# Kernel optimization log

Hardware: AMD Instinct MI355X
Metric: run time of the kernel (lower is better)

## Reference

```python
import jax, jax.numpy as jnp
import numpy as np

N_QUBITS = 16
REPS = 2
BATCH = 512


def _apply_1q_batched(state, gates, q):
    """Apply per-sample 2x2 gates [B,2,2] to qubit q of state [B]+[2]*n."""
    state = jnp.moveaxis(state, 1 + q, -1)
    state = jnp.einsum('bij,b...j->b...i', gates, state)
    return jnp.moveaxis(state, -1, 1 + q)


def _apply_1q(state, gate, q):
    """Apply a shared 2x2 gate to qubit q of state [B]+[2]*n."""
    state = jnp.moveaxis(state, 1 + q, -1)
    state = jnp.einsum('ij,b...j->b...i', gate, state)
    return jnp.moveaxis(state, -1, 1 + q)


def _apply_cnot(state, c, t):
    """CNOT with control c, target t on state [B]+[2]*n."""
    state = jnp.moveaxis(state, (1 + c, 1 + t), (-2, -1))
    state = jnp.stack([state[..., 0, :], state[..., 1, ::-1]], axis=-2)
    return jnp.moveaxis(state, (-2, -1), (1 + c, 1 + t))


def _rx_gates(theta):
    """RX(theta) gates; theta [...,] -> gates [...,2,2] complex64."""
    c = jnp.cos(theta / 2).astype(jnp.complex64)
    s = (-1j * jnp.sin(theta / 2)).astype(jnp.complex64)
    row0 = jnp.stack([c, s], axis=-1)
    row1 = jnp.stack([s, c], axis=-1)
    return jnp.stack([row0, row1], axis=-2)


def _pauliz_signs(n):
    idx = np.arange(2 ** n)
    # pennylane convention: wire 0 is the most significant bit
    bits = (idx[None, :] >> (n - 1 - np.arange(n)[:, None])) & 1  # [n, 2^n]
    return jnp.asarray(1.0 - 2.0 * bits, dtype=jnp.float32)


def setup_inputs() -> dict:
    key = jax.random.key(0)
    kz, kp, kw = jax.random.split(key, 3)
    z = jax.random.normal(kz, (BATCH, N_QUBITS), dtype=jnp.float32)
    params = jax.random.normal(kp, (N_QUBITS,), dtype=jnp.float32) * 0.1
    ent_weights = jax.random.normal(kw, (REPS, N_QUBITS), dtype=jnp.float32) * 0.1
    return {"z": z, "params": params, "ent_weights": ent_weights}


def reference(z, params, ent_weights):
    B, n = z.shape
    # |0...0> initial state, batched
    state = jnp.zeros((B, 2 ** n), dtype=jnp.complex64).at[:, 0].set(1.0)
    state = state.reshape([B] + [2] * n)

    # Embedding layer: RX(z[b,i] + params[i]) on each wire (per-sample angles)
    angles = z + params[None, :]  # [B, n]
    for q in range(n):
        state = _apply_1q_batched(state, _rx_gates(angles[:, q]), q)

    # BasicEntanglerLayers, reps=2: per layer, RX(w) on each wire then ring CNOTs
    for l in range(REPS):
        for q in range(n):
            state = _apply_1q(state, _rx_gates(ent_weights[l, q]), q)
        for q in range(n):
            state = _apply_cnot(state, q, (q + 1) % n)

    # <Z_i> for each wire
    probs = jnp.abs(state.reshape(B, -1)) ** 2  # [B, 2^n] float32
    signs = _pauliz_signs(n)  # [n, 2^n]
    return probs @ signs.T  # [B, n]
```

## Files before the change

kernel.cpp:

```cpp
#include <hip/hip_runtime.h>

#define NQ 16

__device__ __forceinline__ float2 phase_val(float mag, int k) {
    switch (k & 3) {
        case 0:  return make_float2(mag, 0.f);
        case 1:  return make_float2(0.f, -mag);
        case 2:  return make_float2(-mag, 0.f);
        default: return make_float2(0.f, mag);
    }
}

extern "C" __global__ __launch_bounds__(256)
void qsim_kernel(const float* __restrict__ z,
                 const float* __restrict__ params,
                 const float* __restrict__ ew,
                 float* __restrict__ out)
{
    const int b   = blockIdx.x;
    const int tid = threadIdx.x;

    __shared__ float c1[NQ], s1[NQ], cw[NQ], sw[NQ];
    __shared__ float2 V[8][256];
    __shared__ float2 G[2][9][10];

    if (tid < NQ) {
        float phi = z[b * NQ + tid] + params[tid] + ew[tid];
        c1[tid] = cosf(0.5f * phi);
        s1[tid] = sinf(0.5f * phi);
        float w = 0.5f * ew[NQ + tid];
        cw[tid] = cosf(w);
        sw[tid] = sinf(w);
    }
    __syncthreads();

    {
        const int h = tid;
        int y[8];
#pragma unroll
        for (int q = 0; q < 8; ++q) y[q] = (h >> (7 - q)) & 1;

        float2 A[2];
#pragma unroll
        for (int t = 0; t < 2; ++t) {
            float mag = 1.f; int k = 0;
            int e = y[0] ^ t;          mag *= e ? s1[0] : c1[0]; k += e;
            e = y[1] ^ y[0] ^ t;       mag *= e ? s1[1] : c1[1]; k += e;
#pragma unroll
            for (int q = 2; q < 8; ++q) { e = y[q - 1] ^ y[q]; mag *= e ? s1[q] : c1[q]; k += e; }
            A[t] = phase_val(mag, k);
        }
        const int a_act = h & 1;
        V[2 * a_act + 0][h] = A[0];
        V[2 * a_act + 1][h] = A[1];
        V[2 * (1 - a_act) + 0][h] = make_float2(0.f, 0.f);
        V[2 * (1 - a_act) + 1][h] = make_float2(0.f, 0.f);

        float2 Bv[2];
#pragma unroll
        for (int a = 0; a < 2; ++a) {
            float mag = 1.f; int k = 0;
            int e = a ^ y[0];          mag *= e ? s1[8] : c1[8]; k += e;
#pragma unroll
            for (int q = 9; q < 16; ++q) { e = y[q - 9] ^ y[q - 8]; mag *= e ? s1[q] : c1[q]; k += e; }
            Bv[a] = phase_val(mag, k);
        }
        const int b_act = h & 1;
        V[4 + 0 + b_act][h] = Bv[0];
        V[4 + 2 + b_act][h] = Bv[1];
        V[4 + 0 + (1 - b_act)][h] = make_float2(0.f, 0.f);
        V[4 + 2 + (1 - b_act)][h] = make_float2(0.f, 0.f);
    }
    __syncthreads();

    for (int j = 0; j < 8; ++j) {
        const int bit = 7 - j;
#pragma unroll
        for (int r = 0; r < 4; ++r) {
            int task = tid + 256 * r;
            int vec  = task >> 7;
            int pr   = task & 127;
            int h0 = ((pr >> bit) << (bit + 1)) | (pr & ((1 << bit) - 1));
            int h1 = h0 | (1 << bit);
            int wire = (vec < 4) ? j : (8 + j);
            float c = cw[wire], s = sw[wire];
            float2 v0 = V[vec][h0], v1 = V[vec][h1];
            float2 n0 = make_float2(c * v0.x + s * v1.y, c * v0.y - s * v1.x);
            float2 n1 = make_float2(s * v0.y + c * v1.x, -s * v0.x + c * v1.y);
            V[vec][h0] = n0;
            V[vec][h1] = n1;
        }
        __syncthreads();
    }

    if (tid < 180) {
        int side = tid / 90;
        int rest = tid - side * 90;
        int pp   = rest / 9;
        int m    = rest - pp * 9;
        int p, q2;
        if (pp < 4)      { p = 0; q2 = pp; }
        else if (pp < 7) { p = 1; q2 = pp - 3; }
        else if (pp < 9) { p = 2; q2 = pp - 5; }
        else             { p = 3; q2 = 3; }
        int mask;
        if (side == 0) mask = (m < 8) ? (((1 << (m + 1)) - 1) << (7 - m)) : 0x7F;
        else           mask = (m == 0) ? 0 : (((1 << m) - 1) << (8 - m));
        const float2* Vp = V[p  + 4 * side];
        const float2* Vq = V[q2 + 4 * side];
        float ar = 0.f, ai = 0.f;
        for (int e2 = 0; e2 < 256; ++e2) {
            float2 u = Vp[e2], w = Vq[e2];
            float re = u.x * w.x + u.y * w.y;
            float im = u.y * w.x - u.x * w.y;
            float sgn = (__popc(mask & e2) & 1) ? -1.f : 1.f;
            ar = fmaf(sgn, re, ar);
            ai = fmaf(sgn, im, ai);
        }
        G[side][m][pp] = make_float2(ar, ai);
    }
    __syncthreads();

    if (tid < NQ) {
        const int i = tid;
        int hm, lm;
        if (i == 0)      { hm = 8; lm = 8; }
        else if (i <= 7) { hm = i; lm = 0; }
        else             { hm = 7; lm = i - 7; }
        float r = 0.f;
#pragma unroll
        for (int pp = 0; pp < 10; ++pp) {
            float2 gh = G[0][hm][pp];
            float2 gl = G[1][lm][pp];
            float re = gh.x * gl.x - gh.y * gl.y;
            bool diag = (pp == 0) || (pp == 4) || (pp == 7) || (pp == 9);
            r += (diag ? 1.f : 2.f) * re;
        }
        out[b * NQ + i] = r;
    }
}

extern "C" void kernel_launch(void* const* d_in, const int* in_sizes, int n_in,
                              void* d_out, int out_size, void* d_ws, size_t ws_size,
                              hipStream_t stream) {
    const float* z      = (const float*)d_in[0];
    const float* params = (const float*)d_in[1];
    const float* ew     = (const float*)d_in[2];
    float* out          = (float*)d_out;
    const int B = in_sizes[0] / NQ;
    qsim_kernel<<<B, 256, 0, stream>>>(z, params, ew, out);
}
```

Before: 73.21 us.

## Keep state in registers with wave shuffles and use Walsh-Hadamard butterflies for Gram sums

The per-wire RX mixing now runs in registers using wave shuffles instead of shared-memory passes with a barrier after each wire. Only the last wire goes through shared memory via float4 loads. The old 180-thread serial 256-element signed Gram reduction is replaced by an in-register signed butterfly across lanes (a Walsh-Hadamard-style transform). Each wave writes a few partial sums to shared memory, and a small final pass combines them. This removes most barriers and the long serial reduction loops, at the cost of heavier register use (a 32-float array per thread plus many shuffles).

```diff
diff --git a/kernel.cpp b/kernel.cpp
--- a/kernel.cpp
+++ b/kernel.cpp
@@ -11,17 +11,24 @@
     }
 }
 
+__device__ __forceinline__ float2 rxmix(float2 v0, float2 v1, float c, float s) {
+    return make_float2(c * v0.x + s * v1.y, c * v0.y - s * v1.x);
+}
+
 extern "C" __global__ __launch_bounds__(256)
 void qsim_kernel(const float* __restrict__ z,
                  const float* __restrict__ params,
                  const float* __restrict__ ew,
                  float* __restrict__ out)
 {
-    const int b   = blockIdx.x;
-    const int tid = threadIdx.x;
+    const int b    = blockIdx.x;
+    const int tid  = threadIdx.x;
+    const int lane = tid & 63;
+    const int wv   = tid >> 6;
 
     __shared__ float c1[NQ], s1[NQ], cw[NQ], sw[NQ];
-    __shared__ float2 V[8][256];
+    __shared__ __align__(16) float2 V4[4][258];
+    __shared__ __align__(16) float  PART[4][7][32];
     __shared__ float2 G[2][9][10];
 
     if (tid < NQ) {
@@ -34,90 +41,189 @@
     }
     __syncthreads();
 
-    {
-        const int h = tid;
-        int y[8];
-#pragma unroll
-        for (int q = 0; q < 8; ++q) y[q] = (h >> (7 - q)) & 1;
-
-        float2 A[2];
-#pragma unroll
-        for (int t = 0; t < 2; ++t) {
-            float mag = 1.f; int k = 0;
-            int e = y[0] ^ t;          mag *= e ? s1[0] : c1[0]; k += e;
-            e = y[1] ^ y[0] ^ t;       mag *= e ? s1[1] : c1[1]; k += e;
-#pragma unroll
-            for (int q = 2; q < 8; ++q) { e = y[q - 1] ^ y[q]; mag *= e ? s1[q] : c1[q]; k += e; }
-            A[t] = phase_val(mag, k);
-        }
-        const int a_act = h & 1;
-        V[2 * a_act + 0][h] = A[0];
-        V[2 * a_act + 1][h] = A[1];
-        V[2 * (1 - a_act) + 0][h] = make_float2(0.f, 0.f);
-        V[2 * (1 - a_act) + 1][h] = make_float2(0.f, 0.f);
-
-        float2 Bv[2];
-#pragma unroll
-        for (int a = 0; a < 2; ++a) {
-            float mag = 1.f; int k = 0;
-            int e = a ^ y[0];          mag *= e ? s1[8] : c1[8]; k += e;
-#pragma unroll
-            for (int q = 9; q < 16; ++q) { e = y[q - 9] ^ y[q - 8]; mag *= e ? s1[q] : c1[q]; k += e; }
-            Bv[a] = phase_val(mag, k);
-        }
-        const int b_act = h & 1;
-        V[4 + 0 + b_act][h] = Bv[0];
-        V[4 + 2 + b_act][h] = Bv[1];
-        V[4 + 0 + (1 - b_act)][h] = make_float2(0.f, 0.f);
-        V[4 + 2 + (1 - b_act)][h] = make_float2(0.f, 0.f);
-    }
-    __syncthreads();
-
-    for (int j = 0; j < 8; ++j) {
-        const int bit = 7 - j;
-#pragma unroll
-        for (int r = 0; r < 4; ++r) {
-            int task = tid + 256 * r;
-            int vec  = task >> 7;
-            int pr   = task & 127;
-            int h0 = ((pr >> bit) << (bit + 1)) | (pr & ((1 << bit) - 1));
-            int h1 = h0 | (1 << bit);
-            int wire = (vec < 4) ? j : (8 + j);
-            float c = cw[wire], s = sw[wire];
-            float2 v0 = V[vec][h0], v1 = V[vec][h1];
-            float2 n0 = make_float2(c * v0.x + s * v1.y, c * v0.y - s * v1.x);
-            float2 n1 = make_float2(s * v0.y + c * v1.x, -s * v0.x + c * v1.y);
-            V[vec][h0] = n0;
-            V[vec][h1] = n1;
-        }
-        __syncthreads();
-    }
+    const bool hiw = (wv < 2);
+    const int  par = wv & 1;
+
+    float2 v[4];
+#pragma unroll
+    for (int k = 0; k < 4; ++k) {
+        int e = (k << 6) | lane;
+        float mag = 1.f; int kk = 0;
+        if (hiw) {
+            int y0 = (e >> 7) & 1;
+            int eb = y0 ^ par;                 mag *= eb ? s1[0] : c1[0]; kk += eb;
+            int y1 = (e >> 6) & 1;
+            eb = y1 ^ y0 ^ par;                mag *= eb ? s1[1] : c1[1]; kk += eb;
+            int yp = y1;
+#pragma unroll
+            for (int q = 2; q < 8; ++q) {
+                int yq = (e >> (7 - q)) & 1;
+                eb = yp ^ yq;                  mag *= eb ? s1[q] : c1[q]; kk += eb;
+                yp = yq;
+            }
+        } else {
+            int yp = (e >> 7) & 1;
+            int eb = par ^ yp;                 mag *= eb ? s1[8] : c1[8]; kk += eb;
+#pragma unroll
+            for (int q = 9; q < 16; ++q) {
+                int yq = (e >> (15 - q)) & 1;
+                eb = yp ^ yq;                  mag *= eb ? s1[q] : c1[q]; kk += eb;
+                yp = yq;
+            }
+        }
+        v[k] = phase_val(mag, kk);
+    }
+
+    const int wb = hiw ? 0 : 8;
+    {
+        float c = cw[wb + 0], s = sw[wb + 0];
+        float2 n0 = rxmix(v[0], v[2], c, s), n2 = rxmix(v[2], v[0], c, s);
+        float2 n1 = rxmix(v[1], v[3], c, s), n3 = rxmix(v[3], v[1], c, s);
+        v[0] = n0; v[1] = n1; v[2] = n2; v[3] = n3;
+    }
+    {
+        float c = cw[wb + 1], s = sw[wb + 1];
+        float2 n0 = rxmix(v[0], v[1], c, s), n1 = rxmix(v[1], v[0], c, s);
+        float2 n2 = rxmix(v[2], v[3], c, s), n3 = rxmix(v[3], v[2], c, s);
+        v[0] = n0; v[1] = n1; v[2] = n2; v[3] = n3;
+    }
+#pragma unroll
+    for (int bbit = 5; bbit >= 1; --bbit) {
+        float c = cw[wb + 7 - bbit], s = sw[wb + 7 - bbit];
+        int m = 1 << bbit;
+#pragma unroll
+        for (int k = 0; k < 4; ++k) {
+            float px = __shfl_xor(v[k].x, m);
+            float py = __shfl_xor(v[k].y, m);
+            v[k] = make_float2(c * v[k].x + s * py, c * v[k].y - s * px);
+        }
+    }
+#pragma unroll
+    for (int k = 0; k < 4; ++k) V4[wv][(k << 6) | lane] = v[k];
+    __syncthreads();
+
+    const int e0 = tid & 1, j2 = tid & ~1;
+    float4 rA0 = *(const float4*)&V4[0][j2];
+    float4 rA1 = *(const float4*)&V4[1][j2];
+    float4 rB0 = *(const float4*)&V4[2][j2];
+    float4 rB1 = *(const float4*)&V4[3][j2];
+    float c7 = cw[7], s7 = sw[7], c15 = cw[15], s15 = sw[15];
+
+    float2 x[4], yv[4];
+    {
+        float2 a0 = make_float2(rA0.x, rA0.y), b0 = make_float2(rA0.z, rA0.w);
+        float2 a1 = make_float2(rA1.x, rA1.y), b1 = make_float2(rA1.z, rA1.w);
+        if (e0 == 0) {
+            x[0] = make_float2(c7 * a0.x, c7 * a0.y);
+            x[1] = make_float2(c7 * a1.x, c7 * a1.y);
+            x[2] = make_float2(s7 * b0.y, -s7 * b0.x);
+            x[3] = make_float2(s7 * b1.y, -s7 * b1.x);
+        } else {
+            x[0] = make_float2(s7 * a0.y, -s7 * a0.x);
+            x[1] = make_float2(s7 * a1.y, -s7 * a1.x);
+            x[2] = make_float2(c7 * b0.x, c7 * b0.y);
+            x[3] = make_float2(c7 * b1.x, c7 * b1.y);
+        }
+        float2 g0 = make_float2(rB0.x, rB0.y), d0 = make_float2(rB0.z, rB0.w);
+        float2 g1 = make_float2(rB1.x, rB1.y), d1 = make_float2(rB1.z, rB1.w);
+        if (e0 == 0) {
+            yv[0] = make_float2(c15 * g0.x, c15 * g0.y);
+            yv[2] = make_float2(c15 * g1.x, c15 * g1.y);
+            yv[1] = make_float2(s15 * d0.y, -s15 * d0.x);
+            yv[3] = make_float2(s15 * d1.y, -s15 * d1.x);
+        } else {
+            yv[0] = make_float2(s15 * g0.y, -s15 * g0.x);
+            yv[2] = make_float2(s15 * g1.y, -s15 * g1.x);
+            yv[1] = make_float2(c15 * d0.x, c15 * d0.y);
+            yv[3] = make_float2(c15 * d1.x, c15 * d1.y);
+        }
+    }
+
+    float wr[32];
+    {
+        float2 *p = x;
+#pragma unroll
+        for (int side = 0; side < 2; ++side, p = yv) {
+            int o = side * 16;
+            wr[o + 0] = p[0].x * p[0].x + p[0].y * p[0].y;
+            wr[o + 1] = p[1].x * p[1].x + p[1].y * p[1].y;
+            wr[o + 2] = p[2].x * p[2].x + p[2].y * p[2].y;
+            wr[o + 3] = p[3].x * p[3].x + p[3].y * p[3].y;
+            wr[o + 4]  = p[0].x * p[1].x + p[0].y * p[1].y;
+            wr[o + 5]  = p[0].y * p[1].x - p[0].x * p[1].y;
+            wr[o + 6]  = p[0].x * p[2].x + p[0].y * p[2].y;
+            wr[o + 7]  = p[0].y * p[2].x - p[0].x * p[2].y;
+            wr[o + 8]  = p[0].x * p[3].x + p[0].y * p[3].y;
+            wr[o + 9]  = p[0].y * p[3].x - p[0].x * p[3].y;
+            wr[o + 10] = p[1].x * p[2].x + p[1].y * p[2].y;
+            wr[o + 11] = p[1].y * p[2].x - p[1].x * p[2].y;
+            wr[o + 12] = p[1].x * p[3].x + p[1].y * p[3].y;
+            wr[o + 13] = p[1].y * p[3].x - p[1].x * p[3].y;
+            wr[o + 14] = p[2].x * p[3].x + p[2].y * p[3].y;
+            wr[o + 15] = p[2].y * p[3].x - p[2].x * p[3].y;
+        }
+    }
+
+#pragma unroll
+    for (int lev = 0; lev < 6; ++lev) {
+        int m = 1 << lev;
+        float s = (lane & m) ? -1.f : 1.f;
+#pragma unroll
+        for (int a = 0; a < 32; ++a) {
+            float wp = __shfl_xor(wr[a], m);
+            wr[a] = fmaf(s, wr[a], wp);
+        }
+    }
+    {
+        int li = -1;
+        switch (lane) {
+            case 0x00: li = 0; break; case 0x20: li = 1; break;
+            case 0x30: li = 2; break; case 0x38: li = 3; break;
+            case 0x3C: li = 4; break; case 0x3E: li = 5; break;
+            case 0x3F: li = 6; break;
+        }
+        if (li >= 0) {
+#pragma unroll
+            for (int a = 0; a < 32; ++a) PART[wv][li][a] = wr[a];
+        }
+    }
+    __syncthreads();
 
     if (tid < 180) {
-        int side = tid / 90;
-        int rest = tid - side * 90;
-        int pp   = rest / 9;
-        int m    = rest - pp * 9;
-        int p, q2;
-        if (pp < 4)      { p = 0; q2 = pp; }
-        else if (pp < 7) { p = 1; q2 = pp - 3; }
-        else if (pp < 9) { p = 2; q2 = pp - 5; }
-        else             { p = 3; q2 = 3; }
-        int mask;
-        if (side == 0) mask = (m < 8) ? (((1 << (m + 1)) - 1) << (7 - m)) : 0x7F;
-        else           mask = (m == 0) ? 0 : (((1 << m) - 1) << (8 - m));
-        const float2* Vp = V[p  + 4 * side];
-        const float2* Vq = V[q2 + 4 * side];
-        float ar = 0.f, ai = 0.f;
-        for (int e2 = 0; e2 < 256; ++e2) {
-            float2 u = Vp[e2], w = Vq[e2];
-            float re = u.x * w.x + u.y * w.y;
-            float im = u.y * w.x - u.x * w.y;
-            float sgn = (__popc(mask & e2) & 1) ? -1.f : 1.f;
-            ar = fmaf(sgn, re, ar);
-            ai = fmaf(sgn, im, ai);
-        }
-        G[side][m][pp] = make_float2(ar, ai);
+        int side = tid / 90, rest = tid - side * 90;
+        int pp = rest / 9, m = rest - pp * 9;
+        int M;
+        if (side == 0) M = (m < 8) ? (((1 << (m + 1)) - 1) << (7 - m)) : 0x7F;
+        else           M = (m == 0) ? 0 : (((1 << m) - 1) << (8 - m));
+        int low = M & 63, hi2 = M >> 6;
+        int li2 = 0;
+        switch (low) {
+            case 0x00: li2 = 0; break; case 0x20: li2 = 1; break;
+            case 0x30: li2 = 2; break; case 0x38: li2 = 3; break;
+            case 0x3C: li2 = 4; break; case 0x3E: li2 = 5; break;
+            default:   li2 = 6; break;
+        }
+        int rs; bool diag;
+        switch (pp) {
+            case 0: rs = 0;  diag = true;  break;
+            case 1: rs = 4;  diag = false; break;
+            case 2: rs = 6;  diag = false; break;
+            case 3: rs = 8;  diag = false; break;
+            case 4: rs = 1;  diag = true;  break;
+            case 5: rs = 10; diag = false; break;
+            case 6: rs = 12; diag = false; break;
+            case 7: rs = 2;  diag = true;  break;
+            case 8: rs = 14; diag = false; break;
+            default: rs = 3; diag = true;  break;
+        }
+        float gr = 0.f, gi = 0.f;
+#pragma unroll
+        for (int w2 = 0; w2 < 4; ++w2) {
+            float s = (__popc(hi2 & w2) & 1) ? -1.f : 1.f;
+            gr = fmaf(s, PART[w2][li2][side * 16 + rs], gr);
+            if (!diag) gi = fmaf(s, PART[w2][li2][side * 16 + rs + 1], gi);
+        }
+        G[side][m][pp] = make_float2(gr, gi);
     }
     __syncthreads();
 
```

Result: faster. 64.98 us (-11.2%).
